# Optimization experiments

Measured on AMD Instinct MI355X. Metric: run time of the kernel, lower is better.

Reference implementation:

```python
import jax
jax.config.update("jax_enable_x64", True)  # FNV64 needs uint64
import jax.numpy as jnp
import numpy as np

FNV_OFFSET = np.uint64(14695981039346656037)
FNV_PRIME = np.uint64(1099511628211)


def fnv_hash(coords):
    # FNV64-1A over columns, matching fnv_hash_vec
    arr = coords.astype(jnp.uint64)
    h = jnp.full((arr.shape[0],), FNV_OFFSET, dtype=jnp.uint64)
    for j in range(arr.shape[1]):  # fixed small loop over 4 columns
        h = h * FNV_PRIME
        h = jnp.bitwise_xor(h, arr[:, j])
    return h


def setup_inputs() -> dict:
    key = jax.random.key(0)
    k1, k2 = jax.random.split(key)
    N, C = 2_000_000, 16
    coords = jax.random.randint(k1, (N, 4), 0, 48, dtype=jnp.int32)
    feats = jax.random.normal(k2, (N, C), dtype=jnp.float32)
    return {"coords": coords, "feats": feats}


def reference(coords, feats):
    N = coords.shape[0]
    key = fnv_hash(coords)                      # [N] uint64
    idx_sort = jnp.argsort(key)                 # sort by hash (voxel order = hash order)
    key_sort = key[idx_sort]
    # first-occurrence flags in sorted order -> group boundaries (np.unique equivalent)
    first = jnp.concatenate(
        [jnp.ones((1,), bool), key_sort[1:] != key_sort[:-1]])
    group_ids = jnp.cumsum(first.astype(jnp.int32)) - 1  # [N] voxel id per sorted point
    num_voxels = group_ids[-1] + 1              # data-dependent count; outputs padded to N

    feats_sort = feats[idx_sort]
    counts = jax.ops.segment_sum(
        jnp.ones((N,), feats.dtype), group_ids, num_segments=N)
    sums = jax.ops.segment_sum(feats_sort, group_ids, num_segments=N)
    voxel_feats = sums / jnp.maximum(counts, 1.0)[:, None]  # scatter-mean, rows >= num_voxels are zero

    # voxel_coords = coords of first occurrence per group (mask keeps exactly one row per group)
    coords_sort = coords[idx_sort]
    voxel_coords = jax.ops.segment_sum(
        jnp.where(first[:, None], coords_sort, 0), group_ids, num_segments=N)

    # v2p_map = inverse[idx_sort_rev]: voxel id of each original point
    v2p_map = jnp.zeros((N,), jnp.int32).at[idx_sort].set(group_ids)
    return voxel_feats, voxel_coords, v2p_map, num_voxels
```

## Files before the change

### kernel.cpp

```cpp
#include <hip/hip_runtime.h>
#include <vector>
#include <algorithm>
#include <utility>

typedef unsigned long long u64;
typedef unsigned int u32;

#define NTRIP 110592
#define IDXBITS 21
#define IMASK ((1u << IDXBITS) - 1)
#define NCOARSE 512
#define CAPB 5632
#define NSUB 4096
#define PK_E 8
#define PA_E 16
#define SORT_WAVES 4

static u32 g_rank48[NTRIP];
namespace {
struct RankInit {
    RankInit() {
        std::vector<std::pair<u64, u32>> v(NTRIP);
        for (u32 t = 0; t < NTRIP; t++) {
            u64 h = 14695981039346656037ull;
            const u64 P = 1099511628211ull;
            h *= P; h ^= (u64)(t / 2304);
            h *= P; h ^= (u64)((t % 2304) / 48);
            h *= P; h ^= (u64)(t % 48);
            h *= P;
            v[t] = {h, t};
        }
        std::sort(v.begin(), v.end());
        for (u32 p = 0; p < NTRIP; p++)
            g_rank48[v[p].second] = (p << 6) | (u32)(v[p].first & 63ull);
    }
};
static RankInit g_rank_init;
}

__global__ void k_invrank(const u32* __restrict__ rank48, u32* __restrict__ invrank) {
    int tau = blockIdx.x * blockDim.x + threadIdx.x;
    if (tau >= NTRIP) return;
    u32 r = rank48[tau];
    invrank[r >> 6] = ((u32)tau << 6) | (r & 63u);
}

__global__ void k_pkeys(const int* __restrict__ coords, const u32* __restrict__ rank48,
                        u32* __restrict__ hist, u64* __restrict__ pkey64, int N) {
    __shared__ u32 lh[NCOARSE];
    int tid = threadIdx.x;
    for (int d = tid; d < NCOARSE; d += 256) lh[d] = 0;
    __syncthreads();
    int base = blockIdx.x * (256 * PK_E);
#pragma unroll
    for (int k = 0; k < PK_E; k++) {
        int i = base + k * 256 + tid;
        if (i < N) {
            int4 c = ((const int4*)coords)[i];
            u32 tau = (u32)c.x * 2304u + (u32)c.y * 48u + (u32)c.z;
            u32 kk = rank48[tau] ^ (u32)c.w;
            pkey64[i] = ((u64)kk << IDXBITS) | (u32)i;
            atomicAdd(&lh[kk >> 14], 1u);
        }
    }
    __syncthreads();
    for (int d = tid; d < NCOARSE; d += 256)
        if (lh[d]) atomicAdd(&hist[d], lh[d]);
}

__global__ void k_scan512(const u32* __restrict__ in, u32* __restrict__ out,
                          u32* __restrict__ cursor) {
    __shared__ u32 s[256];
    int t = threadIdx.x;
    u32 a = in[2 * t], b = in[2 * t + 1];
    u32 sum = a + b;
    s[t] = sum;
    __syncthreads();
    for (int off = 1; off < 256; off <<= 1) {
        u32 v = (t >= off) ? s[t - off] : 0u;
        __syncthreads();
        s[t] += v;
        __syncthreads();
    }
    u32 tb = s[t] - sum;
    out[2 * t] = tb;
    out[2 * t + 1] = tb + a;
    if (cursor) { cursor[2 * t] = tb; cursor[2 * t + 1] = tb + a; }
    if (t == 255) out[512] = s[255];
}

__global__ void k_passA(const u64* __restrict__ pkey64, u32* __restrict__ cursor,
                        u64* __restrict__ sorted, int N) {
    __shared__ u32 lh[NCOARSE], lclaim[NCOARSE], lcnt[NCOARSE];
    int tid = threadIdx.x;
    for (int d = tid; d < NCOARSE; d += 256) { lh[d] = 0; lcnt[d] = 0; }
    __syncthreads();
    int base = blockIdx.x * (256 * PA_E);
    u64 p[PA_E];
    bool val[PA_E];
#pragma unroll
    for (int k = 0; k < PA_E; k++) {
        int i = base + k * 256 + tid;
        val[k] = i < N;
        p[k] = val[k] ? pkey64[i] : 0;
        if (val[k]) atomicAdd(&lh[(u32)(p[k] >> 35)], 1u);
    }
    __syncthreads();
    for (int d = tid; d < NCOARSE; d += 256) {
        u32 c = lh[d];
        lclaim[d] = c ? atomicAdd(&cursor[d], c) : 0u;
    }
    __syncthreads();
#pragma unroll
    for (int k = 0; k < PA_E; k++) {
        if (val[k]) {
            u32 d = (u32)(p[k] >> 35);
            u32 r = atomicAdd(&lcnt[d], 1u);
            sorted[lclaim[d] + r] = p[k];
        }
    }
}

__global__ __launch_bounds__(256) void k_passB(const u32* __restrict__ base,
                                               u64* __restrict__ sorted,
                                               u32* __restrict__ dcount) {
    __shared__ u64 lout[CAPB];
    __shared__ u32 lbase[NSUB];
    __shared__ u32 lcnt[NSUB];
    __shared__ u32 lpart[256];
    int tid = threadIdx.x;
    int b = blockIdx.x;
    u32 s0 = base[b], s1 = base[b + 1];
    int s = (int)(s1 - s0);
    if (s == 0) { if (tid == 0) dcount[b] = 0; return; }
    if (s > CAPB) {
        if (tid == 0) {
            for (int j = (int)s0 + 1; j < (int)s1; j++) {
                u64 pj = sorted[j];
                int k2 = j - 1;
                while (k2 >= (int)s0 && sorted[k2] > pj) { sorted[k2 + 1] = sorted[k2]; k2--; }
                sorted[k2 + 1] = pj;
            }
            u32 c = 1;
            for (int j = (int)s0 + 1; j < (int)s1; j++)
                c += ((u32)(sorted[j] >> IDXBITS) != (u32)(sorted[j - 1] >> IDXBITS)) ? 1u : 0u;
            dcount[b] = c;
        }
        return;
    }
    for (int d = tid; d < NSUB; d += 256) { lbase[d] = 0; lcnt[d] = 0; }
    __syncthreads();
    u64 p[22];
#pragma unroll
    for (int k = 0; k < 22; k++) {
        int e = k * 256 + tid;
        if (e < s) {
            p[k] = sorted[s0 + e];
            atomicAdd(&lbase[(u32)(p[k] >> 23) & 0xFFFu], 1u);
        }
    }
    __syncthreads();
    u32 mycnt[16];
    u32 run = 0;
#pragma unroll
    for (int k = 0; k < 16; k++) { mycnt[k] = lbase[tid * 16 + k]; run += mycnt[k]; }
    lpart[tid] = run;
    __syncthreads();
    for (int off = 1; off < 256; off <<= 1) {
        u32 v = (tid >= off) ? lpart[tid - off] : 0u;
        __syncthreads();
        lpart[tid] += v;
        __syncthreads();
    }
    u32 tb = lpart[tid] - run;
#pragma unroll
    for (int k = 0; k < 16; k++) { u32 c = mycnt[k]; lbase[tid * 16 + k] = tb; tb += c; }
    __syncthreads();
#pragma unroll
    for (int k = 0; k < 22; k++) {
        int e = k * 256 + tid;
        if (e < s) {
            u32 d = (u32)(p[k] >> 23) & 0xFFFu;
            u32 slot = lbase[d] + atomicAdd(&lcnt[d], 1u);
            lout[slot] = p[k];
        }
    }
    __syncthreads();
    for (int d = tid; d < NSUB; d += 256) {
        u32 c = lcnt[d];
        if (c >= 2) {
            u32 st = lbase[d];
            for (u32 j = st + 1; j < st + c; j++) {
                u64 pj = lout[j];
                int k2 = (int)j - 1;
                while (k2 >= (int)st && lout[k2] > pj) { lout[k2 + 1] = lout[k2]; k2--; }
                lout[k2 + 1] = pj;
            }
        }
    }
    __syncthreads();
    u32 cnt = 0;
    for (int e = tid; e < s; e += 256) {
        u64 pv = lout[e];
        sorted[s0 + e] = pv;
        u32 key = (u32)(pv >> IDXBITS);
        u32 pk = (e == 0) ? 0xFFFFFFFFu : (u32)(lout[e - 1] >> IDXBITS);
        cnt += (key != pk) ? 1u : 0u;
    }
    lpart[tid] = cnt;
    __syncthreads();
    for (int off = 128; off > 0; off >>= 1) {
        if (tid < off) lpart[tid] += lpart[tid + off];
        __syncthreads();
    }
    if (tid == 0) dcount[b] = lpart[0];
}

__global__ void k_emit(const u32* __restrict__ base, const u32* __restrict__ gidbase,
                       const u64* __restrict__ sorted, float* __restrict__ v2p,
                       u32* __restrict__ voxstart, u32* __restrict__ nvslot, int N) {
    int w = threadIdx.x >> 6;
    int lane = threadIdx.x & 63;
    u32 b = blockIdx.x * SORT_WAVES + (u32)w;
    if (b >= NCOARSE) return;
    int start = (int)base[b], end = (int)base[b + 1];
    int s = end - start;
    if (s == 0) return;
    u32 gb = gidbase[b];
    u32 carry = 0;
    u32 prevlast = 0xFFFFFFFFu;
    for (int off = 0; off < s; off += 64) {
        int e = off + lane;
        bool valid = e < s;
        u64 p = valid ? sorted[start + e] : 0;
        u32 key = (u32)(p >> IDXBITS);
        u32 idx = (u32)p & IMASK;
        u32 pk = __shfl_up(key, 1);
        if (lane == 0) pk = (off == 0) ? 0xFFFFFFFFu : prevlast;
        u32 f = (valid && key != pk) ? 1u : 0u;
        u32 pf = f;
        for (int d = 1; d < 64; d <<= 1) {
            u32 t = __shfl_up(pf, d);
            if (lane >= d) pf += t;
        }
        u32 gid = gb + carry + pf - 1u;
        if (valid) {
            v2p[idx] = (float)gid;
            if (f) voxstart[gid] = (u32)(start + e);
            if (start + e == N - 1) { voxstart[gid + 1] = (u32)N; nvslot[0] = gid + 1u; }
        }
        carry += __shfl(pf, 63);
        prevlast = __shfl(key, 63);
    }
}

__global__ void k_vox(const u32* __restrict__ voxstart, const u64* __restrict__ sorted,
                      const u32* __restrict__ invrank, const float* __restrict__ feats,
                      const u32* __restrict__ nvslot, float* __restrict__ vox_feats,
                      float* __restrict__ vox_coords, float* __restrict__ nvox, int N) {
    int t = blockIdx.x * blockDim.x + threadIdx.x;
    if (t >= N) return;
    u32 nv = nvslot[0];
    if (t == 0) nvox[0] = (float)nv;
    if ((u32)t >= nv) {
        float4 z = {0, 0, 0, 0};
        float4* vf = (float4*)(vox_feats + (size_t)t * 16);
        vf[0] = z; vf[1] = z; vf[2] = z; vf[3] = z;
        *(float4*)(vox_coords + (size_t)t * 4) = z;
        return;
    }
    u32 s0 = voxstart[t];
    u32 s1 = voxstart[t + 1];
    u64 p0 = sorted[s0];
    u32 kk = (u32)(p0 >> IDXBITS);
    float4 a0 = {0, 0, 0, 0}, a1 = {0, 0, 0, 0}, a2 = {0, 0, 0, 0}, a3 = {0, 0, 0, 0};
    for (u32 e = s0; e < s1; e++) {
        u32 idx = (u32)sorted[e] & IMASK;
        const float4* f = (const float4*)(feats + (size_t)idx * 16);
        float4 v0 = f[0], v1 = f[1], v2 = f[2], v3 = f[3];
        a0.x += v0.x; a0.y += v0.y; a0.z += v0.z; a0.w += v0.w;
        a1.x += v1.x; a1.y += v1.y; a1.z += v1.z; a1.w += v1.w;
        a2.x += v2.x; a2.y += v2.y; a2.z += v2.z; a2.w += v2.w;
        a3.x += v3.x; a3.y += v3.y; a3.z += v3.z; a3.w += v3.w;
    }
    float fc = (float)(s1 - s0);
    float4* vf = (float4*)(vox_feats + (size_t)t * 16);
    vf[0] = make_float4(a0.x / fc, a0.y / fc, a0.z / fc, a0.w / fc);
    vf[1] = make_float4(a1.x / fc, a1.y / fc, a1.z / fc, a1.w / fc);
    vf[2] = make_float4(a2.x / fc, a2.y / fc, a2.z / fc, a2.w / fc);
    vf[3] = make_float4(a3.x / fc, a3.y / fc, a3.z / fc, a3.w / fc);
    u32 iv = invrank[kk >> 6];
    u32 tau = iv >> 6;
    u32 c3 = (kk ^ iv) & 63u;
    *(float4*)(vox_coords + (size_t)t * 4) =
        make_float4((float)(tau / 2304u), (float)((tau % 2304u) / 48u),
                    (float)(tau % 48u), (float)c3);
}

extern "C" void kernel_launch(void* const* d_in, const int* in_sizes, int n_in,
                              void* d_out, int out_size, void* d_ws, size_t ws_size,
                              hipStream_t stream) {
    const int* coords = (const int*)d_in[0];
    const float* feats = (const float*)d_in[1];
    int N = in_sizes[0] / 4;

    float* out = (float*)d_out;
    float* vox_feats = out;
    float* vox_coords = out + (size_t)N * 16;
    float* v2p = vox_coords + (size_t)N * 4;
    float* nvox = v2p + (size_t)N;

    char* w = (char*)d_ws;
    u64* pkey64 = (u64*)w;     w += (size_t)N * 8;
    u64* sorted = (u64*)w;     w += (size_t)N * 8;
    u32* hist = (u32*)w;       w += 512 * 4;
    u32* basearr = (u32*)w;    w += 513 * 4;
    u32* cursor = (u32*)w;     w += 512 * 4;
    u32* dcount = (u32*)w;     w += 512 * 4;
    u32* gidbase = (u32*)w;    w += 513 * 4;
    u32* voxstart = (u32*)w;   w += ((size_t)N + 1) * 4;
    u32* rank48_d = (u32*)w;   w += (size_t)NTRIP * 4;
    u32* invrank_d = (u32*)w;  w += (size_t)NTRIP * 4;
    u32* nvslot = (u32*)w;     w += 256;

    hipMemcpyAsync(rank48_d, g_rank48, sizeof(g_rank48), hipMemcpyHostToDevice, stream);
    hipMemsetAsync(hist, 0, 512 * 4, stream);

    int blocksT = (NTRIP + 255) / 256;
    int blocksPK = (N + 256 * PK_E - 1) / (256 * PK_E);
    int blocksPA = (N + 256 * PA_E - 1) / (256 * PA_E);
    int blocksN = (N + 255) / 256;

    k_invrank<<<blocksT, 256, 0, stream>>>(rank48_d, invrank_d);
    k_pkeys<<<blocksPK, 256, 0, stream>>>(coords, rank48_d, hist, pkey64, N);
    k_scan512<<<1, 256, 0, stream>>>(hist, basearr, cursor);
    k_passA<<<blocksPA, 256, 0, stream>>>(pkey64, cursor, sorted, N);
    k_passB<<<NCOARSE, 256, 0, stream>>>(basearr, sorted, dcount);
    k_scan512<<<1, 256, 0, stream>>>(dcount, gidbase, (u32*)nullptr);
    k_emit<<<NCOARSE / SORT_WAVES, 256, 0, stream>>>(basearr, gidbase, sorted, v2p,
                                                     voxstart, nvslot, N);
    k_vox<<<blocksN, 256, 0, stream>>>(voxstart, sorted, invrank_d, feats, nvslot,
                                       vox_feats, vox_coords, nvox, N);
}
```

Baseline: 375.7 us.

## Fuse hashing with bucket scatter and derive voxel ids from an occupancy bitmap

```diff
diff --git a/kernel.cpp b/kernel.cpp
--- a/kernel.cpp
+++ b/kernel.cpp
@@ -12,9 +12,8 @@
 #define NCOARSE 512
 #define CAPB 5632
 #define NSUB 4096
-#define PK_E 8
-#define PA_E 16
-#define SORT_WAVES 4
+#define NWORDS 131072
+#define K1_E 8
 
 static u32 g_rank48[NTRIP];
 namespace {
@@ -45,125 +44,132 @@
     invrank[r >> 6] = ((u32)tau << 6) | (r & 63u);
 }
 
-__global__ void k_pkeys(const int* __restrict__ coords, const u32* __restrict__ rank48,
-                        u32* __restrict__ hist, u64* __restrict__ pkey64, int N) {
-    __shared__ u32 lh[NCOARSE];
-    int tid = threadIdx.x;
-    for (int d = tid; d < NCOARSE; d += 256) lh[d] = 0;
-    __syncthreads();
-    int base = blockIdx.x * (256 * PK_E);
-#pragma unroll
-    for (int k = 0; k < PK_E; k++) {
-        int i = base + k * 256 + tid;
-        if (i < N) {
-            int4 c = ((const int4*)coords)[i];
-            u32 tau = (u32)c.x * 2304u + (u32)c.y * 48u + (u32)c.z;
-            u32 kk = rank48[tau] ^ (u32)c.w;
-            pkey64[i] = ((u64)kk << IDXBITS) | (u32)i;
-            atomicAdd(&lh[kk >> 14], 1u);
-        }
-    }
-    __syncthreads();
-    for (int d = tid; d < NCOARSE; d += 256)
-        if (lh[d]) atomicAdd(&hist[d], lh[d]);
-}
-
-__global__ void k_scan512(const u32* __restrict__ in, u32* __restrict__ out,
-                          u32* __restrict__ cursor) {
-    __shared__ u32 s[256];
-    int t = threadIdx.x;
-    u32 a = in[2 * t], b = in[2 * t + 1];
-    u32 sum = a + b;
-    s[t] = sum;
-    __syncthreads();
-    for (int off = 1; off < 256; off <<= 1) {
-        u32 v = (t >= off) ? s[t - off] : 0u;
-        __syncthreads();
-        s[t] += v;
-        __syncthreads();
-    }
-    u32 tb = s[t] - sum;
-    out[2 * t] = tb;
-    out[2 * t + 1] = tb + a;
-    if (cursor) { cursor[2 * t] = tb; cursor[2 * t + 1] = tb + a; }
-    if (t == 255) out[512] = s[255];
-}
-
-__global__ void k_passA(const u64* __restrict__ pkey64, u32* __restrict__ cursor,
-                        u64* __restrict__ sorted, int N) {
+__global__ void k_hashscatter(const int* __restrict__ coords, const u32* __restrict__ rank48,
+                              u32* __restrict__ fill, u64* __restrict__ bitmap,
+                              u64* __restrict__ sortedp, u32* __restrict__ pkey, int N) {
     __shared__ u32 lh[NCOARSE], lclaim[NCOARSE], lcnt[NCOARSE];
     int tid = threadIdx.x;
     for (int d = tid; d < NCOARSE; d += 256) { lh[d] = 0; lcnt[d] = 0; }
     __syncthreads();
-    int base = blockIdx.x * (256 * PA_E);
-    u64 p[PA_E];
-    bool val[PA_E];
-#pragma unroll
-    for (int k = 0; k < PA_E; k++) {
+    int base = blockIdx.x * (256 * K1_E);
+    u32 kk[K1_E];
+    bool val[K1_E];
+#pragma unroll
+    for (int k = 0; k < K1_E; k++) {
         int i = base + k * 256 + tid;
         val[k] = i < N;
-        p[k] = val[k] ? pkey64[i] : 0;
-        if (val[k]) atomicAdd(&lh[(u32)(p[k] >> 35)], 1u);
+        if (val[k]) {
+            int4 c = ((const int4*)coords)[i];
+            u32 tau = (u32)c.x * 2304u + (u32)c.y * 48u + (u32)c.z;
+            u32 key = rank48[tau] ^ (u32)c.w;
+            kk[k] = key;
+            pkey[i] = key;
+            atomicOr(&bitmap[key >> 6], 1ull << (key & 63u));
+            atomicAdd(&lh[key >> 14], 1u);
+        }
     }
     __syncthreads();
     for (int d = tid; d < NCOARSE; d += 256) {
         u32 c = lh[d];
-        lclaim[d] = c ? atomicAdd(&cursor[d], c) : 0u;
-    }
-    __syncthreads();
-#pragma unroll
-    for (int k = 0; k < PA_E; k++) {
+        lclaim[d] = c ? atomicAdd(&fill[d], c) : 0u;
+    }
+    __syncthreads();
+#pragma unroll
+    for (int k = 0; k < K1_E; k++) {
         if (val[k]) {
-            u32 d = (u32)(p[k] >> 35);
-            u32 r = atomicAdd(&lcnt[d], 1u);
-            sorted[lclaim[d] + r] = p[k];
-        }
-    }
-}
-
-__global__ __launch_bounds__(256) void k_passB(const u32* __restrict__ base,
-                                               u64* __restrict__ sorted,
-                                               u32* __restrict__ dcount) {
+            int i = base + k * 256 + tid;
+            u32 d = kk[k] >> 14;
+            u32 r = lclaim[d] + atomicAdd(&lcnt[d], 1u);
+            if (r < CAPB) sortedp[(size_t)d * CAPB + r] = ((u64)kk[k] << IDXBITS) | (u32)i;
+        }
+    }
+}
+
+__global__ void k_wprefix(const u64* __restrict__ bitmap, u32* __restrict__ wprefix,
+                          u32* __restrict__ dtotal) {
+    __shared__ u32 s[256];
+    int t = threadIdx.x, b = blockIdx.x;
+    int w = b * 256 + t;
+    u32 c = (u32)__popcll(bitmap[w]);
+    s[t] = c;
+    __syncthreads();
+    for (int off = 1; off < 256; off <<= 1) {
+        u32 v = (t >= off) ? s[t - off] : 0u;
+        __syncthreads();
+        s[t] += v;
+        __syncthreads();
+    }
+    wprefix[w] = s[t] - c;
+    if (t == 255) dtotal[b] = s[255];
+}
+
+__global__ void k_meta(const u32* __restrict__ fill, const u32* __restrict__ dtotal,
+                       u32* __restrict__ pointbase, u32* __restrict__ gidbase,
+                       u32* __restrict__ nvslot) {
+    __shared__ u32 s[256];
+    int t = threadIdx.x;
+    u32 f0 = fill[2 * t], f1 = fill[2 * t + 1];
+    u32 a = f0 < CAPB ? f0 : CAPB, b = f1 < CAPB ? f1 : CAPB;
+    u32 sum = a + b;
+    s[t] = sum;
+    __syncthreads();
+    for (int off = 1; off < 256; off <<= 1) {
+        u32 v = (t >= off) ? s[t - off] : 0u;
+        __syncthreads();
+        s[t] += v;
+        __syncthreads();
+    }
+    u32 tb = s[t] - sum;
+    pointbase[2 * t] = tb;
+    pointbase[2 * t + 1] = tb + a;
+    __syncthreads();
+    u32 a2 = dtotal[2 * t], b2 = dtotal[2 * t + 1];
+    u32 sum2 = a2 + b2;
+    s[t] = sum2;
+    __syncthreads();
+    for (int off = 1; off < 256; off <<= 1) {
+        u32 v = (t >= off) ? s[t - off] : 0u;
+        __syncthreads();
+        s[t] += v;
+        __syncthreads();
+    }
+    u32 tb2 = s[t] - sum2;
+    gidbase[2 * t] = tb2;
+    gidbase[2 * t + 1] = tb2 + a2;
+    if (t == 255) nvslot[0] = s[255];
+}
+
+__global__ __launch_bounds__(256) void k_sortbucket(const u32* __restrict__ fill,
+                                                    const u32* __restrict__ pointbase,
+                                                    const u32* __restrict__ gidbase,
+                                                    const u64* __restrict__ sortedp,
+                                                    u32* __restrict__ mlist,
+                                                    u64* __restrict__ voxmeta) {
     __shared__ u64 lout[CAPB];
-    __shared__ u32 lbase[NSUB];
-    __shared__ u32 lcnt[NSUB];
+    __shared__ u32 lbins[NSUB * 2];
     __shared__ u32 lpart[256];
-    int tid = threadIdx.x;
-    int b = blockIdx.x;
-    u32 s0 = base[b], s1 = base[b + 1];
-    int s = (int)(s1 - s0);
-    if (s == 0) { if (tid == 0) dcount[b] = 0; return; }
-    if (s > CAPB) {
-        if (tid == 0) {
-            for (int j = (int)s0 + 1; j < (int)s1; j++) {
-                u64 pj = sorted[j];
-                int k2 = j - 1;
-                while (k2 >= (int)s0 && sorted[k2] > pj) { sorted[k2 + 1] = sorted[k2]; k2--; }
-                sorted[k2 + 1] = pj;
-            }
-            u32 c = 1;
-            for (int j = (int)s0 + 1; j < (int)s1; j++)
-                c += ((u32)(sorted[j] >> IDXBITS) != (u32)(sorted[j - 1] >> IDXBITS)) ? 1u : 0u;
-            dcount[b] = c;
-        }
-        return;
-    }
-    for (int d = tid; d < NSUB; d += 256) { lbase[d] = 0; lcnt[d] = 0; }
+    int tid = threadIdx.x, b = blockIdx.x;
+    u32 fb = fill[b];
+    int s = (int)(fb < CAPB ? fb : CAPB);
+    if (s == 0) return;
+    u32 pb = pointbase[b], gb = gidbase[b];
+    size_t base = (size_t)b * CAPB;
+    for (int d = tid; d < NSUB; d += 256) { lbins[d] = 0; lbins[NSUB + d] = 0; }
     __syncthreads();
     u64 p[22];
 #pragma unroll
     for (int k = 0; k < 22; k++) {
         int e = k * 256 + tid;
         if (e < s) {
-            p[k] = sorted[s0 + e];
-            atomicAdd(&lbase[(u32)(p[k] >> 23) & 0xFFFu], 1u);
-        }
-    }
-    __syncthreads();
-    u32 mycnt[16];
+            p[k] = sortedp[base + e];
+            atomicAdd(&lbins[(u32)(p[k] >> 23) & 0xFFFu], 1u);
+        }
+    }
+    __syncthreads();
+    u32 my[16];
     u32 run = 0;
 #pragma unroll
-    for (int k = 0; k < 16; k++) { mycnt[k] = lbase[tid * 16 + k]; run += mycnt[k]; }
+    for (int k = 0; k < 16; k++) { my[k] = lbins[tid * 16 + k]; run += my[k]; }
     lpart[tid] = run;
     __syncthreads();
     for (int off = 1; off < 256; off <<= 1) {
@@ -174,22 +180,22 @@
     }
     u32 tb = lpart[tid] - run;
 #pragma unroll
-    for (int k = 0; k < 16; k++) { u32 c = mycnt[k]; lbase[tid * 16 + k] = tb; tb += c; }
+    for (int k = 0; k < 16; k++) { u32 c = my[k]; lbins[tid * 16 + k] = tb; tb += c; }
     __syncthreads();
 #pragma unroll
     for (int k = 0; k < 22; k++) {
         int e = k * 256 + tid;
         if (e < s) {
             u32 d = (u32)(p[k] >> 23) & 0xFFFu;
-            u32 slot = lbase[d] + atomicAdd(&lcnt[d], 1u);
+            u32 slot = lbins[d] + atomicAdd(&lbins[NSUB + d], 1u);
             lout[slot] = p[k];
         }
     }
     __syncthreads();
     for (int d = tid; d < NSUB; d += 256) {
-        u32 c = lcnt[d];
+        u32 c = lbins[NSUB + d];
         if (c >= 2) {
-            u32 st = lbase[d];
+            u32 st = lbins[d];
             for (u32 j = st + 1; j < st + c; j++) {
                 u64 pj = lout[j];
                 int k2 = (int)j - 1;
@@ -199,62 +205,56 @@
         }
     }
     __syncthreads();
+    for (int e = tid; e < s; e += 256) mlist[pb + e] = (u32)lout[e] & IMASK;
+    int per = (s + 255) / 256;
+    int e0 = tid * per;
+    int e1 = e0 + per; if (e1 > s) e1 = s;
     u32 cnt = 0;
-    for (int e = tid; e < s; e += 256) {
-        u64 pv = lout[e];
-        sorted[s0 + e] = pv;
-        u32 key = (u32)(pv >> IDXBITS);
-        u32 pk = (e == 0) ? 0xFFFFFFFFu : (u32)(lout[e - 1] >> IDXBITS);
+    for (int e = e0; e < e1; e++) {
+        u32 key = (u32)(lout[e] >> IDXBITS);
+        u32 pk = e ? (u32)(lout[e - 1] >> IDXBITS) : 0xFFFFFFFFu;
         cnt += (key != pk) ? 1u : 0u;
     }
     lpart[tid] = cnt;
     __syncthreads();
-    for (int off = 128; off > 0; off >>= 1) {
-        if (tid < off) lpart[tid] += lpart[tid + off];
-        __syncthreads();
-    }
-    if (tid == 0) dcount[b] = lpart[0];
-}
-
-__global__ void k_emit(const u32* __restrict__ base, const u32* __restrict__ gidbase,
-                       const u64* __restrict__ sorted, float* __restrict__ v2p,
-                       u32* __restrict__ voxstart, u32* __restrict__ nvslot, int N) {
-    int w = threadIdx.x >> 6;
-    int lane = threadIdx.x & 63;
-    u32 b = blockIdx.x * SORT_WAVES + (u32)w;
-    if (b >= NCOARSE) return;
-    int start = (int)base[b], end = (int)base[b + 1];
-    int s = end - start;
-    if (s == 0) return;
-    u32 gb = gidbase[b];
-    u32 carry = 0;
-    u32 prevlast = 0xFFFFFFFFu;
-    for (int off = 0; off < s; off += 64) {
-        int e = off + lane;
-        bool valid = e < s;
-        u64 p = valid ? sorted[start + e] : 0;
-        u32 key = (u32)(p >> IDXBITS);
-        u32 idx = (u32)p & IMASK;
-        u32 pk = __shfl_up(key, 1);
-        if (lane == 0) pk = (off == 0) ? 0xFFFFFFFFu : prevlast;
-        u32 f = (valid && key != pk) ? 1u : 0u;
-        u32 pf = f;
-        for (int d = 1; d < 64; d <<= 1) {
-            u32 t = __shfl_up(pf, d);
-            if (lane >= d) pf += t;
-        }
-        u32 gid = gb + carry + pf - 1u;
-        if (valid) {
-            v2p[idx] = (float)gid;
-            if (f) voxstart[gid] = (u32)(start + e);
-            if (start + e == N - 1) { voxstart[gid + 1] = (u32)N; nvslot[0] = gid + 1u; }
-        }
-        carry += __shfl(pf, 63);
-        prevlast = __shfl(key, 63);
-    }
-}
-
-__global__ void k_vox(const u32* __restrict__ voxstart, const u64* __restrict__ sorted,
+    for (int off = 1; off < 256; off <<= 1) {
+        u32 v = (tid >= off) ? lpart[tid - off] : 0u;
+        __syncthreads();
+        lpart[tid] += v;
+        __syncthreads();
+    }
+    u32 dcnt = lpart[255];
+    u32 g = lpart[tid] - cnt;
+    __syncthreads();
+    u32* starts = lbins;
+    for (int e = e0; e < e1; e++) {
+        u32 key = (u32)(lout[e] >> IDXBITS);
+        u32 pk = e ? (u32)(lout[e - 1] >> IDXBITS) : 0xFFFFFFFFu;
+        if (key != pk) starts[g++] = (u32)e;
+    }
+    __syncthreads();
+    for (u32 L = tid; L < dcnt; L += 256) {
+        u32 st = starts[L];
+        u32 en = (L + 1 < dcnt) ? starts[L + 1] : (u32)s;
+        u32 key = (u32)(lout[st] >> IDXBITS);
+        u32 c = en - st; if (c > 511u) c = 511u;
+        voxmeta[gb + L] = (u64)(pb + st) | ((u64)key << 32) | ((u64)c << 55);
+    }
+}
+
+__global__ void k_v2p(const u32* __restrict__ pkey, const u64* __restrict__ bitmap,
+                      const u32* __restrict__ wprefix, const u32* __restrict__ gidbase,
+                      float* __restrict__ v2p, int N) {
+    int i = blockIdx.x * blockDim.x + threadIdx.x;
+    if (i >= N) return;
+    u32 kk = pkey[i];
+    u64 word = bitmap[kk >> 6];
+    u32 gid = gidbase[kk >> 14] + wprefix[kk >> 6] +
+              (u32)__popcll(word & ((1ull << (kk & 63u)) - 1ull));
+    v2p[i] = (float)gid;
+}
+
+__global__ void k_vox(const u64* __restrict__ voxmeta, const u32* __restrict__ mlist,
                       const u32* __restrict__ invrank, const float* __restrict__ feats,
                       const u32* __restrict__ nvslot, float* __restrict__ vox_feats,
                       float* __restrict__ vox_coords, float* __restrict__ nvox, int N) {
@@ -269,13 +269,13 @@
         *(float4*)(vox_coords + (size_t)t * 4) = z;
         return;
     }
-    u32 s0 = voxstart[t];
-    u32 s1 = voxstart[t + 1];
-    u64 p0 = sorted[s0];
-    u32 kk = (u32)(p0 >> IDXBITS);
+    u64 m = voxmeta[t];
+    u32 st = (u32)m;
+    u32 kk = (u32)(m >> 32) & 0x7FFFFFu;
+    u32 c = (u32)(m >> 55);
     float4 a0 = {0, 0, 0, 0}, a1 = {0, 0, 0, 0}, a2 = {0, 0, 0, 0}, a3 = {0, 0, 0, 0};
-    for (u32 e = s0; e < s1; e++) {
-        u32 idx = (u32)sorted[e] & IMASK;
+    for (u32 e = st; e < st + c; e++) {
+        u32 idx = mlist[e];
         const float4* f = (const float4*)(feats + (size_t)idx * 16);
         float4 v0 = f[0], v1 = f[1], v2 = f[2], v3 = f[3];
         a0.x += v0.x; a0.y += v0.y; a0.z += v0.z; a0.w += v0.w;
@@ -283,7 +283,7 @@
         a2.x += v2.x; a2.y += v2.y; a2.z += v2.z; a2.w += v2.w;
         a3.x += v3.x; a3.y += v3.y; a3.z += v3.z; a3.w += v3.w;
     }
-    float fc = (float)(s1 - s0);
+    float fc = (float)c;
     float4* vf = (float4*)(vox_feats + (size_t)t * 16);
     vf[0] = make_float4(a0.x / fc, a0.y / fc, a0.z / fc, a0.w / fc);
     vf[1] = make_float4(a1.x / fc, a1.y / fc, a1.z / fc, a1.w / fc);
@@ -311,34 +311,35 @@
     float* nvox = v2p + (size_t)N;
 
     char* w = (char*)d_ws;
-    u64* pkey64 = (u64*)w;     w += (size_t)N * 8;
-    u64* sorted = (u64*)w;     w += (size_t)N * 8;
-    u32* hist = (u32*)w;       w += 512 * 4;
-    u32* basearr = (u32*)w;    w += 513 * 4;
-    u32* cursor = (u32*)w;     w += 512 * 4;
-    u32* dcount = (u32*)w;     w += 512 * 4;
-    u32* gidbase = (u32*)w;    w += 513 * 4;
-    u32* voxstart = (u32*)w;   w += ((size_t)N + 1) * 4;
+    u64* sortedp = (u64*)w;    w += (size_t)NCOARSE * CAPB * 8;
+    u32* pkey = (u32*)w;       w += (size_t)N * 4;
+    u32* mlist = (u32*)w;      w += (size_t)N * 4;
+    u64* voxmeta = (u64*)w;    w += (size_t)N * 8;
+    u64* bitmap = (u64*)w;     w += (size_t)NWORDS * 8;
+    u32* fill = (u32*)w;       w += NCOARSE * 4;
+    u32* wprefix = (u32*)w;    w += (size_t)NWORDS * 4;
+    u32* dtotal = (u32*)w;     w += NCOARSE * 4;
+    u32* pointbase = (u32*)w;  w += NCOARSE * 4;
+    u32* gidbase = (u32*)w;    w += NCOARSE * 4;
     u32* rank48_d = (u32*)w;   w += (size_t)NTRIP * 4;
     u32* invrank_d = (u32*)w;  w += (size_t)NTRIP * 4;
     u32* nvslot = (u32*)w;     w += 256;
 
     hipMemcpyAsync(rank48_d, g_rank48, sizeof(g_rank48), hipMemcpyHostToDevice, stream);
-    hipMemsetAsync(hist, 0, 512 * 4, stream);
+    hipMemsetAsync(bitmap, 0, (size_t)NWORDS * 8 + NCOARSE * 4, stream);
 
     int blocksT = (NTRIP + 255) / 256;
-    int blocksPK = (N + 256 * PK_E - 1) / (256 * PK_E);
-    int blocksPA = (N + 256 * PA_E - 1) / (256 * PA_E);
+    int blocksK1 = (N + 256 * K1_E - 1) / (256 * K1_E);
     int blocksN = (N + 255) / 256;
 
     k_invrank<<<blocksT, 256, 0, stream>>>(rank48_d, invrank_d);
-    k_pkeys<<<blocksPK, 256, 0, stream>>>(coords, rank48_d, hist, pkey64, N);
-    k_scan512<<<1, 256, 0, stream>>>(hist, basearr, cursor);
-    k_passA<<<blocksPA, 256, 0, stream>>>(pkey64, cursor, sorted, N);
-    k_passB<<<NCOARSE, 256, 0, stream>>>(basearr, sorted, dcount);
-    k_scan512<<<1, 256, 0, stream>>>(dcount, gidbase, (u32*)nullptr);
-    k_emit<<<NCOARSE / SORT_WAVES, 256, 0, stream>>>(basearr, gidbase, sorted, v2p,
-                                                     voxstart, nvslot, N);
-    k_vox<<<blocksN, 256, 0, stream>>>(voxstart, sorted, invrank_d, feats, nvslot,
+    k_hashscatter<<<blocksK1, 256, 0, stream>>>(coords, rank48_d, fill, bitmap,
+                                                sortedp, pkey, N);
+    k_wprefix<<<NCOARSE, 256, 0, stream>>>(bitmap, wprefix, dtotal);
+    k_meta<<<1, 256, 0, stream>>>(fill, dtotal, pointbase, gidbase, nvslot);
+    k_sortbucket<<<NCOARSE, 256, 0, stream>>>(fill, pointbase, gidbase, sortedp,
+                                              mlist, voxmeta);
+    k_v2p<<<blocksN, 256, 0, stream>>>(pkey, bitmap, wprefix, gidbase, v2p, N);
+    k_vox<<<blocksN, 256, 0, stream>>>(voxmeta, mlist, invrank_d, feats, nvslot,
                                        vox_feats, vox_coords, nvox, N);
 }
```

New measurement: 384.1 us. 1.02x slower.
